# Kernel tuning notes

Hardware: AMD Instinct MI355X
Metric: run time of the kernel (lower is better)

The kernel has to match this reference:

```python
import jax, jax.numpy as jnp
import numpy as np

H = 128; W = 128; WH = 8; WW = 8; SH = 4; SW = 4
DIM = 512; HEADS = 16; HD = DIM // HEADS; HIDDEN = 2048
NH = H // WH; NW = W // WW; NWIN = NH * NW; WL = WH * WW
EPS = 1e-5
SCALE = HD ** -0.5


def _rel_pos_index():
    # Swin-style relative position index, static (WL, WL) int table
    coords = np.stack(np.meshgrid(np.arange(WH), np.arange(WW), indexing='ij')).reshape(2, -1)
    rel = (coords[:, :, None] - coords[:, None, :]).transpose(1, 2, 0)  # (WL, WL, 2)
    rel[:, :, 0] += WH - 1
    rel[:, :, 1] += WW - 1
    rel[:, :, 0] *= 2 * WW - 1
    return rel.sum(-1)  # (WL, WL), values in [0, (2WH-1)(2WW-1))


def _shift_attn_mask():
    # static shifted-window attention mask, (NWIN, WL, WL)
    m = np.zeros((H, W))
    cnt = 0
    for hs in (slice(0, -WH), slice(-WH, -SH), slice(-SH, None)):
        for ws in (slice(0, -WW), slice(-WW, -SW), slice(-SW, None)):
            m[hs, ws] = cnt
            cnt += 1
    mw = m.reshape(NH, WH, NW, WW).transpose(0, 2, 1, 3).reshape(NWIN, WL)
    am = mw[:, None, :] - mw[:, :, None]
    return np.where(am != 0, -100.0, 0.0).astype(np.float32)


_RPI = _rel_pos_index()
_MASK = _shift_attn_mask()


def _layernorm(x, w, b):
    mu = x.mean(-1, keepdims=True)
    var = ((x - mu) ** 2).mean(-1, keepdims=True)
    return (x - mu) / jnp.sqrt(var + EPS) * w + b


def _win_part(x):  # (H, W, D) -> (NWIN, WL, D)
    return x.reshape(NH, WH, NW, WW, DIM).transpose(0, 2, 1, 3, 4).reshape(NWIN, WL, DIM)


def _win_rev(w):  # (NWIN, WL, D) -> (H, W, D)
    return w.reshape(NH, NW, WH, WW, DIM).transpose(0, 2, 1, 3, 4).reshape(H, W, DIM)


def setup_inputs() -> dict:
    key = jax.random.key(0)
    ks = jax.random.split(key, 8)
    s = 0.02
    return {
        'x': jax.random.normal(ks[0], (H * W, DIM), dtype=jnp.float32),
        'ln1_w': jnp.ones((DIM,), jnp.float32),
        'ln1_b': jnp.zeros((DIM,), jnp.float32),
        'ln2_w': jnp.ones((DIM,), jnp.float32),
        'ln2_b': jnp.zeros((DIM,), jnp.float32),
        'qkv_w': jax.random.normal(ks[1], (3 * DIM, DIM), dtype=jnp.float32) * s,
        'qkv_b': jnp.zeros((3 * DIM,), jnp.float32),
        'proj_w': jax.random.normal(ks[2], (DIM, DIM), dtype=jnp.float32) * s,
        'proj_b': jnp.zeros((DIM,), jnp.float32),
        'rpb': jax.random.normal(ks[3], ((2 * WH - 1) * (2 * WW - 1), HEADS), dtype=jnp.float32) * s,
        'mlp_w1': jax.random.normal(ks[4], (HIDDEN, DIM), dtype=jnp.float32) * s,
        'mlp_b1': jnp.zeros((HIDDEN,), jnp.float32),
        'mlp_w2': jax.random.normal(ks[5], (DIM, HIDDEN), dtype=jnp.float32) * s,
        'mlp_b2': jnp.zeros((DIM,), jnp.float32),
    }


def reference(x, ln1_w, ln1_b, ln2_w, ln2_b, qkv_w, qkv_b, proj_w, proj_b, rpb,
              mlp_w1, mlp_b1, mlp_w2, mlp_b2):
    skip = x
    h = _layernorm(x, ln1_w, ln1_b).reshape(H, W, DIM)
    # cyclic shift + window partition
    h = jnp.roll(h, shift=(-SH, -SW), axis=(0, 1))
    xw = _win_part(h)  # (NWIN, WL, DIM)
    # windowed multi-head self-attention (equinox Linear: y = W @ x + b)
    qkv = jnp.einsum('nld,ed->nle', xw, qkv_w) + qkv_b
    q, k, v = [t.reshape(NWIN, WL, HEADS, HD).transpose(0, 2, 1, 3)
               for t in jnp.split(qkv, 3, axis=-1)]  # each (NWIN, HEADS, WL, HD)
    attn = jnp.einsum('nhqd,nhkd->nhqk', q * SCALE, k)
    bias = rpb[_RPI.reshape(-1)].reshape(WL, WL, HEADS).transpose(2, 0, 1)  # (HEADS, WL, WL)
    attn = attn + bias[None] + jnp.asarray(_MASK)[:, None]
    attn = jax.nn.softmax(attn, axis=-1)
    out = jnp.einsum('nhqk,nhkd->nhqd', attn, v).transpose(0, 2, 1, 3).reshape(NWIN, WL, DIM)
    out = jnp.einsum('nld,ed->nle', out, proj_w) + proj_b
    # window reverse + reverse cyclic shift
    h = jnp.roll(_win_rev(out), shift=(SH, SW), axis=(0, 1)).reshape(H * W, DIM)
    h = skip + h  # residual (drop_path is Identity at rate 0)
    # FFN branch (note: original code does x = x + drop_path(x), i.e. 2*mlp(norm2(.)))
    h = _layernorm(h, ln2_w, ln2_b)
    m = jax.nn.gelu(jnp.einsum('ld,ed->le', h, mlp_w1) + mlp_b1)
    m = jnp.einsum('le,de->ld', m, mlp_w2) + mlp_b2
    return m + m
```

## Files before the change

kernel.cpp:

```cpp
#include <hip/hip_runtime.h>
#include <hip/hip_bf16.h>
#include <stdint.h>

#define TOK   16384
#define DIMM  512
#define NHEAD 16
#define HDIM  32
#define HID   2048
#define NWIN  256
#define WLEN  64
#define EPSV  1e-5f
#define SCL   0.17677669529663687f

typedef __hip_bfloat16 bf16;
typedef __attribute__((ext_vector_type(8))) __bf16 bf16x8;
typedef __attribute__((ext_vector_type(4))) float f32x4;

__device__ __forceinline__ int remap_row(int r){
  int win = r >> 6, l = r & 63;
  int gh = ((win >> 4) << 3) + (l >> 3);
  int gw = ((win & 15) << 3) + (l & 7);
  int oh = (gh + 4) & 127, ow = (gw + 4) & 127;
  return (oh << 7) + ow;
}

__device__ __forceinline__ int region_of(int win, int l){
  int gh = ((win >> 4) << 3) + (l >> 3);
  int gw = ((win & 15) << 3) + (l & 7);
  int rh = (gh < 120) ? 0 : ((gh < 124) ? 1 : 2);
  int rw = (gw < 120) ? 0 : ((gw < 124) ? 1 : 2);
  return rh * 3 + rw;
}

__device__ __forceinline__ void gl_lds16(const bf16* g, bf16* l){
  __builtin_amdgcn_global_load_lds((const __attribute__((address_space(1))) void*)g,
                                   (__attribute__((address_space(3))) void*)l, 16, 0, 0);
}

__global__ __launch_bounds__(256) void convert_w(const float* __restrict__ a,
                                                 const float* __restrict__ b,
                                                 const float* __restrict__ c,
                                                 const float* __restrict__ d,
                                                 bf16* __restrict__ dst){
  int e = (blockIdx.x * 256 + threadIdx.x) * 4;
  float4 v;
  if (e < 786432)        v = *(const float4*)(a + e);
  else if (e < 1048576)  v = *(const float4*)(b + (e - 786432));
  else if (e < 2097152)  v = *(const float4*)(c + (e - 1048576));
  else                   v = *(const float4*)(d + (e - 2097152));
  union { bf16 h[4]; int2 q; } u;
  u.h[0] = __float2bfloat16(v.x); u.h[1] = __float2bfloat16(v.y);
  u.h[2] = __float2bfloat16(v.z); u.h[3] = __float2bfloat16(v.w);
  *(int2*)(dst + e) = u.q;
}

template<bool REMAP>
__global__ __launch_bounds__(256) void ln_kernel(const float* __restrict__ in,
    const float* __restrict__ w, const float* __restrict__ b, bf16* __restrict__ outp)
{
  const int wave = threadIdx.x >> 6, lane = threadIdx.x & 63;
  const int r = blockIdx.x * 4 + wave;
  const int src = REMAP ? remap_row(r) : r;
  const float4* row = (const float4*)(in + (size_t)src * DIMM);
  float4 v0 = row[lane*2], v1 = row[lane*2 + 1];
  float sm = v0.x+v0.y+v0.z+v0.w + v1.x+v1.y+v1.z+v1.w;
  float sq = v0.x*v0.x+v0.y*v0.y+v0.z*v0.z+v0.w*v0.w
           + v1.x*v1.x+v1.y*v1.y+v1.z*v1.z+v1.w*v1.w;
  #pragma unroll
  for (int off = 1; off < 64; off <<= 1){
    sm += __shfl_xor(sm, off);
    sq += __shfl_xor(sq, off);
  }
  const float mean = sm * (1.f/512.f);
  const float rstd = rsqrtf(sq*(1.f/512.f) - mean*mean + EPSV);
  const float4* wp = (const float4*)w; const float4* bp = (const float4*)b;
  float4 w0 = wp[lane*2], w1 = wp[lane*2+1], b0 = bp[lane*2], b1 = bp[lane*2+1];
  union { bf16 h[8]; int4 q; } u;
  u.h[0] = __float2bfloat16((v0.x-mean)*rstd*w0.x + b0.x);
  u.h[1] = __float2bfloat16((v0.y-mean)*rstd*w0.y + b0.y);
  u.h[2] = __float2bfloat16((v0.z-mean)*rstd*w0.z + b0.z);
  u.h[3] = __float2bfloat16((v0.w-mean)*rstd*w0.w + b0.w);
  u.h[4] = __float2bfloat16((v1.x-mean)*rstd*w1.x + b1.x);
  u.h[5] = __float2bfloat16((v1.y-mean)*rstd*w1.y + b1.y);
  u.h[6] = __float2bfloat16((v1.z-mean)*rstd*w1.z + b1.z);
  u.h[7] = __float2bfloat16((v1.w-mean)*rstd*w1.w + b1.w);
  *(int4*)(outp + (size_t)r*DIMM + lane*8) = u.q;
}

#define M_QKV  0
#define M_PROJ 1
#define M_MLP1 2
#define M_MLP2 3
#define M_PART 4

template<int MODE, int K>
__global__ __launch_bounds__(256) void gemm_bt(const bf16* __restrict__ A,
    const bf16* __restrict__ Wt, const float* __restrict__ bias,
    bf16* __restrict__ out_b, float* __restrict__ out_f, const float* __restrict__ skip)
{
  __shared__ bf16 lsA[2][128*32];
  __shared__ bf16 lsB[2][128*32];
  const int tid = threadIdx.x, wave = tid >> 6, lane = tid & 63;
  const int lrow = lane & 15, lgrp = lane >> 4;
  const int m0 = blockIdx.x * 128, n0 = blockIdx.y * 128;
  const int wr = (wave >> 1) * 64, wc = (wave & 1) * 64;

  f32x4 acc[4][4] = {};

  const bf16* Abase = A  + (size_t)m0 * K;
  const bf16* Bbase = Wt + (size_t)n0 * K;
  const int srow = tid >> 2;
  const int scol = (tid & 3) * 8;

  #define STAGE(kt, bf) { \
    gl_lds16(Abase + (size_t)(srow)      * K + (kt) + scol, lsA[bf] + wave*512); \
    gl_lds16(Abase + (size_t)(srow + 64) * K + (kt) + scol, lsA[bf] + 2048 + wave*512); \
    gl_lds16(Bbase + (size_t)(srow)      * K + (kt) + scol, lsB[bf] + wave*512); \
    gl_lds16(Bbase + (size_t)(srow + 64) * K + (kt) + scol, lsB[bf] + 2048 + wave*512); \
  }

  STAGE(0, 0);
  __syncthreads();
  int cur = 0;
  for (int kt = 0; kt < K; kt += 32){
    if (kt + 32 < K) STAGE(kt + 32, cur ^ 1);
    bf16x8 af[4], bfv[4];
    #pragma unroll
    for (int i = 0; i < 4; i++){
      af[i]  = *(const bf16x8*)(lsA[cur] + (wr + i*16 + lrow)*32 + lgrp*8);
      bfv[i] = *(const bf16x8*)(lsB[cur] + (wc + i*16 + lrow)*32 + lgrp*8);
    }
    #pragma unroll
    for (int i = 0; i < 4; i++)
      #pragma unroll
      for (int j = 0; j < 4; j++)
        acc[i][j] = __builtin_amdgcn_mfma_f32_16x16x32_bf16(af[i], bfv[j], acc[i][j], 0, 0, 0);
    __syncthreads();
    cur ^= 1;
  }
  #undef STAGE

  #pragma unroll
  for (int i = 0; i < 4; i++){
    #pragma unroll
    for (int j = 0; j < 4; j++){
      const int col   = n0 + wc + j*16 + lrow;
      const int row_b = m0 + wr + i*16 + lgrp*4;
      const float bv = bias[col];
      #pragma unroll
      for (int rr = 0; rr < 4; rr++){
        const int row = row_b + rr;
        float v = acc[i][j][rr] + bv;
        if constexpr (MODE == M_PROJ){
          const int o = remap_row(row);
          out_f[(size_t)o*DIMM + col] = v + skip[(size_t)o*DIMM + col];
        } else {
          out_f[(size_t)row*DIMM + col] = v;
        }
      }
    }
  }
}

template<int KSTR>
__device__ __forceinline__ void stage_ht(const bf16* __restrict__ P,
                                         int grow0, bf16* lbase, int tid, int kt){
  const int r = tid >> 3;
  const int c = ((tid & 7) ^ (r & 7)) * 8;
  const bf16* g = P + (size_t)(grow0 + r) * KSTR + kt * 64 + c;
  bf16* l = lbase + r * 64 + (tid & 7) * 8;
  gl_lds16(g, l);
  gl_lds16(g + (size_t)64 * KSTR, l + 4096);
}

template<int MODE, int KEXT, int KSTR = KEXT>
__global__ __launch_bounds__(512, 2) void gemm8_bt(const bf16* __restrict__ A,
    const bf16* __restrict__ Wt, const float* __restrict__ bias,
    bf16* __restrict__ out_b, float* __restrict__ out_f, float* __restrict__ out_f2)
{
  constexpr int NT = KEXT / 64;
  extern __shared__ bf16 lds[];
  bf16* As = lds;
  bf16* Bs = lds + 32768;
  const int tid = threadIdx.x;
  const int ln = tid & 63, wv = tid >> 6;
  const int lrow = ln & 15, lgrp = ln >> 4;
  const int swz = lrow & 7;
  const int wm = wv >> 2, wn = wv & 3;
  const int m0 = blockIdx.x * 256, n0 = blockIdx.y * 256;

  if constexpr (MODE == M_PART){
    const int z = blockIdx.z;
    A  += z * 1024;
    Wt += z * 1024;
  }

  f32x4 acc[8][4] = {};
  bf16x8 aA[4][2], bB0[2][2], bB1[2][2];

  #define LDA(MH) { _Pragma("unroll") for (int mf = 0; mf < 4; mf++) \
    _Pragma("unroll") for (int ks = 0; ks < 2; ks++) \
      aA[mf][ks] = *(const bf16x8*)(As + s*16384 + (wm*128 + (MH)*64 + mf*16 + lrow)*64 + ((ks*4 + lgrp) ^ swz)*8); }
  #define LDB(DST, NH) { _Pragma("unroll") for (int nf = 0; nf < 2; nf++) \
    _Pragma("unroll") for (int ks = 0; ks < 2; ks++) \
      DST[nf][ks] = *(const bf16x8*)(Bs + s*16384 + (wn*64 + (NH)*32 + nf*16 + lrow)*64 + ((ks*4 + lgrp) ^ swz)*8); }
  #define QUAD(BARR, IM0, JN0) { _Pragma("unroll") for (int ks = 0; ks < 2; ks++) \
    _Pragma("unroll") for (int mf = 0; mf < 4; mf++) \
      _Pragma("unroll") for (int nf = 0; nf < 2; nf++) \
        acc[(IM0)+mf][(JN0)+nf] = __builtin_amdgcn_mfma_f32_16x16x32_bf16(aA[mf][ks], BARR[nf][ks], acc[(IM0)+mf][(JN0)+nf], 0, 0, 0); }
  #define SBAR() { __builtin_amdgcn_sched_barrier(0); __builtin_amdgcn_s_barrier(); __builtin_amdgcn_sched_barrier(0); }
  #define LGKM0() { asm volatile("s_waitcnt lgkmcnt(0)" ::: "memory"); __builtin_amdgcn_sched_barrier(0); }

  stage_ht<KSTR>(A,  m0,       As,        tid, 0);
  stage_ht<KSTR>(Wt, n0,       Bs,        tid, 0);
  stage_ht<KSTR>(Wt, n0 + 128, Bs + 8192, tid, 0);
  stage_ht<KSTR>(A,  m0 + 128, As + 8192, tid, 0);
  asm volatile("s_waitcnt vmcnt(0)" ::: "memory");
  SBAR();
  stage_ht<KSTR>(Wt, n0,       Bs + 16384,        tid, 1);
  stage_ht<KSTR>(A,  m0,       As + 16384,        tid, 1);
  stage_ht<KSTR>(Wt, n0 + 128, Bs + 16384 + 8192, tid, 1);

  for (int t = 0; t < NT; ++t){
    const int s = t & 1;
    const int sx = s ^ 1;
    LDA(0); LDB(bB0, 0);
    if (t + 1 < NT) stage_ht<KSTR>(A, m0 + 128, As + sx*16384 + 8192, tid, t + 1);
    SBAR(); LGKM0();
    __builtin_amdgcn_s_setprio(1); QUAD(bB0, 0, 0); __builtin_amdgcn_s_setprio(0);
    SBAR();
    LDB(bB1, 1);
    SBAR(); LGKM0();
    __builtin_amdgcn_s_setprio(1); QUAD(bB1, 0, 2); __builtin_amdgcn_s_setprio(0);
    SBAR();
    LDA(1);
    if (t + 2 < NT) stage_ht<KSTR>(Wt, n0, Bs + s*16384, tid, t + 2);
    SBAR(); LGKM0();
    __builtin_amdgcn_s_setprio(1); QUAD(bB1, 4, 2); __builtin_amdgcn_s_setprio(0);
    SBAR();
    if (t + 2 < NT){
      stage_ht<KSTR>(A,  m0,       As + s*16384,        tid, t + 2);
      stage_ht<KSTR>(Wt, n0 + 128, Bs + s*16384 + 8192, tid, t + 2);
    }
    SBAR();
    __builtin_amdgcn_s_setprio(1); QUAD(bB0, 4, 0); __builtin_amdgcn_s_setprio(0);
    if (t == NT - 2)      { asm volatile("s_waitcnt vmcnt(0)" ::: "memory"); }
    else if (t < NT - 2)  { asm volatile("s_waitcnt vmcnt(6)" ::: "memory"); }
    SBAR();
  }
  #undef LDA
  #undef LDB
  #undef QUAD
  #undef SBAR
  #undef LGKM0

  float* pdst = nullptr;
  if constexpr (MODE == M_PART) pdst = blockIdx.z ? out_f2 : out_f;
  #pragma unroll
  for (int im = 0; im < 8; im++){
    #pragma unroll
    for (int jn = 0; jn < 4; jn++){
      const int col = n0 + wn*64 + (jn >> 1)*32 + (jn & 1)*16 + lrow;
      const int row_b = m0 + wm*128 + (im >> 2)*64 + (im & 3)*16 + lgrp*4;
      const float bv = (MODE == M_PART) ? 0.f : bias[col];
      #pragma unroll
      for (int rr = 0; rr < 4; rr++){
        const int row = row_b + rr;
        float v = acc[im][jn][rr] + bv;
        if constexpr (MODE == M_QKV){
          const int t = col >> 9, rem = col & 511;
          const int head = rem >> 5, hd = rem & 31;
          const int win = row >> 6, l = row & 63;
          out_b[(size_t)t * (TOK*DIMM) + ((size_t)(win*NHEAD + head)*WLEN + l)*HDIM + hd]
              = __float2bfloat16(v);
        } else if constexpr (MODE == M_MLP1){
          const float u = 1.5957691216057308f * (v + 0.044715f*v*v*v);
          const float g = v * (1.0f / (1.0f + __expf(-u)));
          out_b[(size_t)row*HID + col] = __float2bfloat16(g);
        } else if constexpr (MODE == M_PART){
          pdst[(size_t)row*DIMM + col] = v;
        } else {
          out_f[(size_t)row*DIMM + col] = 2.f * v;
        }
      }
    }
  }
}

__global__ __launch_bounds__(256) void mlp2_reduce(const float* __restrict__ p0,
    float* __restrict__ dout, const float* __restrict__ bias){
  const int i = blockIdx.x * 256 + threadIdx.x;
  const int e = i * 4;
  float4 a = *(const float4*)(p0 + e);
  float4 b = *(const float4*)(dout + e);
  float4 bv = *(const float4*)(bias + (e & 511));
  float4 r;
  r.x = 2.f*(a.x + b.x + bv.x);
  r.y = 2.f*(a.y + b.y + bv.y);
  r.z = 2.f*(a.z + b.z + bv.z);
  r.w = 2.f*(a.w + b.w + bv.w);
  *(float4*)(dout + e) = r;
}

__global__ __launch_bounds__(256) void attn_kernel(const bf16* __restrict__ qkv,
    const float* __restrict__ rpb, bf16* __restrict__ outp)
{
  __shared__ bf16 Pl[4][64][72];
  const int wave = threadIdx.x >> 6, lane = threadIdx.x & 63;
  const int lrow = lane & 15, lgrp = lane >> 4;
  const int wh = blockIdx.x * 4 + wave;
  const int win = wh >> 4, head = wh & 15;
  const bf16* qb = qkv + (size_t)wh * (WLEN*HDIM);
  const bf16* kb = qb + (size_t)TOK * DIMM;
  const bf16* vb = kb + (size_t)TOK * DIMM;

  bf16x8 aq[4], ak[4];
  #pragma unroll
  for (int i = 0; i < 4; i++){
    aq[i] = *(const bf16x8*)(qb + (i*16 + lrow)*HDIM + lgrp*8);
    ak[i] = *(const bf16x8*)(kb + (i*16 + lrow)*HDIM + lgrp*8);
  }
  f32x4 s[4][4] = {};
  #pragma unroll
  for (int i = 0; i < 4; i++)
    #pragma unroll
    for (int j = 0; j < 4; j++)
      s[i][j] = __builtin_amdgcn_mfma_f32_16x16x32_bf16(aq[i], ak[j], s[i][j], 0, 0, 0);

  #pragma unroll
  for (int i = 0; i < 4; i++){
    #pragma unroll
    for (int rr = 0; rr < 4; rr++){
      const int srow = i*16 + lgrp*4 + rr;
      const int rq = region_of(win, srow);
      float vals[4]; float mx = -1e30f;
      #pragma unroll
      for (int j = 0; j < 4; j++){
        const int scol = j*16 + lrow;
        const int idx = ((srow>>3) - (scol>>3) + 7)*15 + ((srow&7) - (scol&7) + 7);
        float v = s[i][j][rr]*SCL + rpb[idx*NHEAD + head];
        if (region_of(win, scol) != rq) v -= 100.f;
        vals[j] = v; mx = fmaxf(mx, v);
      }
      mx = fmaxf(mx, __shfl_xor(mx, 1));
      mx = fmaxf(mx, __shfl_xor(mx, 2));
      mx = fmaxf(mx, __shfl_xor(mx, 4));
      mx = fmaxf(mx, __shfl_xor(mx, 8));
      float sum = 0.f;
      #pragma unroll
      for (int j = 0; j < 4; j++){ vals[j] = __expf(vals[j] - mx); sum += vals[j]; }
      sum += __shfl_xor(sum, 1); sum += __shfl_xor(sum, 2);
      sum += __shfl_xor(sum, 4); sum += __shfl_xor(sum, 8);
      const float rs = 1.f / sum;
      #pragma unroll
      for (int j = 0; j < 4; j++)
        Pl[wave][srow][j*16 + lrow] = __float2bfloat16(vals[j] * rs);
    }
  }

  f32x4 o[4][2] = {};
  const __bf16* vraw = (const __bf16*)vb;
  #pragma unroll
  for (int st = 0; st < 2; st++){
    bf16x8 pa[4];
    #pragma unroll
    for (int i = 0; i < 4; i++)
      pa[i] = *(const bf16x8*)(&Pl[wave][i*16 + lrow][st*32 + lgrp*8]);
    bf16x8 bv[2];
    #pragma unroll
    for (int j = 0; j < 2; j++){
      #pragma unroll
      for (int jj = 0; jj < 8; jj++)
        bv[j][jj] = vraw[(size_t)(st*32 + lgrp*8 + jj)*HDIM + j*16 + lrow];
    }
    #pragma unroll
    for (int i = 0; i < 4; i++)
      #pragma unroll
      for (int j = 0; j < 2; j++)
        o[i][j] = __builtin_amdgcn_mfma_f32_16x16x32_bf16(pa[i], bv[j], o[i][j], 0, 0, 0);
  }
  bf16* orow = outp + (size_t)win * WLEN * DIMM + head * HDIM;
  #pragma unroll
  for (int i = 0; i < 4; i++)
    #pragma unroll
    for (int j = 0; j < 2; j++)
      #pragma unroll
      for (int rr = 0; rr < 4; rr++){
        const int l = i*16 + lgrp*4 + rr;
        orow[(size_t)l * DIMM + j*16 + lrow] = __float2bfloat16(o[i][j][rr]);
      }
}

extern "C" void kernel_launch(void* const* d_in, const int* in_sizes, int n_in,
                              void* d_out, int out_size, void* d_ws, size_t ws_size,
                              hipStream_t stream) {
  const float* x     = (const float*)d_in[0];
  const float* ln1w  = (const float*)d_in[1];
  const float* ln1b  = (const float*)d_in[2];
  const float* ln2w  = (const float*)d_in[3];
  const float* ln2b  = (const float*)d_in[4];
  const float* qkvw  = (const float*)d_in[5];
  const float* qkvbi = (const float*)d_in[6];
  const float* projw = (const float*)d_in[7];
  const float* projb = (const float*)d_in[8];
  const float* rpb   = (const float*)d_in[9];
  const float* m1w   = (const float*)d_in[10];
  const float* m1b   = (const float*)d_in[11];
  const float* m2w   = (const float*)d_in[12];
  const float* m2b   = (const float*)d_in[13];

  bf16* wqkv  = (bf16*)d_ws;
  bf16* wproj = wqkv + 786432;
  bf16* wm1   = wproj + 262144;
  bf16* wm2   = wm1 + 1048576;
  bf16* xw    = wm2 + 1048576;
  float* hbuf = (float*)(xw + 8388608);
  bf16* qkvb  = (bf16*)(hbuf + 8388608);
  bf16* attno = qkvb + 3*(size_t)8388608;
  bf16* m1buf = qkvb;
  bf16* h2    = xw;

  hipFuncSetAttribute((const void*)&gemm8_bt<M_QKV, 512>,
                      hipFuncAttributeMaxDynamicSharedMemorySize, 131072);
  hipFuncSetAttribute((const void*)&gemm8_bt<M_MLP1, 512>,
                      hipFuncAttributeMaxDynamicSharedMemorySize, 131072);
  hipFuncSetAttribute((const void*)&gemm8_bt<M_PART, 1024, 2048>,
                      hipFuncAttributeMaxDynamicSharedMemorySize, 131072);

  convert_w<<<3072, 256, 0, stream>>>(qkvw, projw, m1w, m2w, wqkv);
  ln_kernel<true><<<4096, 256, 0, stream>>>(x, ln1w, ln1b, xw);
  { dim3 g(TOK/256, 1536/256);
    gemm8_bt<M_QKV, 512><<<g, 512, 131072, stream>>>(xw, wqkv, qkvbi, qkvb, nullptr, nullptr); }
  attn_kernel<<<1024, 256, 0, stream>>>(qkvb, rpb, attno);
  { dim3 g(TOK/128, 512/128);
    gemm_bt<M_PROJ, 512><<<g, 256, 0, stream>>>(attno, wproj, projb, nullptr, hbuf, x); }
  ln_kernel<false><<<4096, 256, 0, stream>>>(hbuf, ln2w, ln2b, h2);
  { dim3 g(TOK/256, 2048/256);
    gemm8_bt<M_MLP1, 512><<<g, 512, 131072, stream>>>(h2, wm1, m1b, m1buf, nullptr, nullptr); }
  { dim3 g(TOK/256, 512/256, 2);
    gemm8_bt<M_PART, 1024, 2048><<<g, 512, 131072, stream>>>(m1buf, wm2, m2b, nullptr,
                                                             hbuf, (float*)d_out); }
  mlp2_reduce<<<8388608/4/256, 256, 0, stream>>>(hbuf, (float*)d_out, m2b);
}
```

Baseline: 229.6 us.

## Store MLP2 split-K partials in bf16 and drop redundant GEMM barriers

The split-K partial sums of the second MLP GEMM are now written as bf16 into scratch buffers instead of fp32, and the reduce kernel reads two bf16 partials and writes fp32 output. This roughly halves the partial-write and reduce-read traffic at the cost of precision in the partial sums. Separately, several workgroup barriers before the LDS-wait/MFMA sections in the gemm8 main loop are removed to cut synchronisation stalls. Removing those barriers risks LDS races if the remaining barriers do not fully order staging against reads.

```diff
diff --git a/kernel.cpp b/kernel.cpp
--- a/kernel.cpp
+++ b/kernel.cpp
@@ -226,23 +226,22 @@
     const int sx = s ^ 1;
     LDA(0); LDB(bB0, 0);
     if (t + 1 < NT) stage_ht<KSTR>(A, m0 + 128, As + sx*16384 + 8192, tid, t + 1);
-    SBAR(); LGKM0();
+    LGKM0();
     __builtin_amdgcn_s_setprio(1); QUAD(bB0, 0, 0); __builtin_amdgcn_s_setprio(0);
     SBAR();
     LDB(bB1, 1);
-    SBAR(); LGKM0();
+    LGKM0();
     __builtin_amdgcn_s_setprio(1); QUAD(bB1, 0, 2); __builtin_amdgcn_s_setprio(0);
     SBAR();
     LDA(1);
     if (t + 2 < NT) stage_ht<KSTR>(Wt, n0, Bs + s*16384, tid, t + 2);
-    SBAR(); LGKM0();
+    LGKM0();
     __builtin_amdgcn_s_setprio(1); QUAD(bB1, 4, 2); __builtin_amdgcn_s_setprio(0);
     SBAR();
     if (t + 2 < NT){
       stage_ht<KSTR>(A,  m0,       As + s*16384,        tid, t + 2);
       stage_ht<KSTR>(Wt, n0 + 128, Bs + s*16384 + 8192, tid, t + 2);
     }
-    SBAR();
     __builtin_amdgcn_s_setprio(1); QUAD(bB0, 4, 0); __builtin_amdgcn_s_setprio(0);
     if (t == NT - 2)      { asm volatile("s_waitcnt vmcnt(0)" ::: "memory"); }
     else if (t < NT - 2)  { asm volatile("s_waitcnt vmcnt(6)" ::: "memory"); }
@@ -254,8 +253,9 @@
   #undef SBAR
   #undef LGKM0
 
-  float* pdst = nullptr;
-  if constexpr (MODE == M_PART) pdst = blockIdx.z ? out_f2 : out_f;
+  bf16* pdstb = nullptr;
+  if constexpr (MODE == M_PART)
+    pdstb = blockIdx.z ? (bf16*)out_f2 : (bf16*)out_f;
   #pragma unroll
   for (int im = 0; im < 8; im++){
     #pragma unroll
@@ -278,7 +278,7 @@
           const float g = v * (1.0f / (1.0f + __expf(-u)));
           out_b[(size_t)row*HID + col] = __float2bfloat16(g);
         } else if constexpr (MODE == M_PART){
-          pdst[(size_t)row*DIMM + col] = v;
+          pdstb[(size_t)row*DIMM + col] = __float2bfloat16(v);
         } else {
           out_f[(size_t)row*DIMM + col] = 2.f * v;
         }
@@ -287,19 +287,27 @@
   }
 }
 
-__global__ __launch_bounds__(256) void mlp2_reduce(const float* __restrict__ p0,
-    float* __restrict__ dout, const float* __restrict__ bias){
-  const int i = blockIdx.x * 256 + threadIdx.x;
-  const int e = i * 4;
-  float4 a = *(const float4*)(p0 + e);
-  float4 b = *(const float4*)(dout + e);
-  float4 bv = *(const float4*)(bias + (e & 511));
-  float4 r;
-  r.x = 2.f*(a.x + b.x + bv.x);
-  r.y = 2.f*(a.y + b.y + bv.y);
-  r.z = 2.f*(a.z + b.z + bv.z);
-  r.w = 2.f*(a.w + b.w + bv.w);
-  *(float4*)(dout + e) = r;
+__global__ __launch_bounds__(256) void mlp2_reduce(const bf16* __restrict__ p0,
+    const bf16* __restrict__ p1, float* __restrict__ dout, const float* __restrict__ bias){
+  const size_t i = (size_t)(blockIdx.x * 256 + threadIdx.x) * 8;
+  int4 a = *(const int4*)(p0 + i);
+  int4 b = *(const int4*)(p1 + i);
+  const int cb = (int)(i & 511);
+  const float4 bv0 = *(const float4*)(bias + cb);
+  const float4 bv1 = *(const float4*)(bias + cb + 4);
+  const bf16* ah = (const bf16*)&a;
+  const bf16* bh = (const bf16*)&b;
+  float4 r0, r1;
+  r0.x = 2.f*(__bfloat162float(ah[0]) + __bfloat162float(bh[0]) + bv0.x);
+  r0.y = 2.f*(__bfloat162float(ah[1]) + __bfloat162float(bh[1]) + bv0.y);
+  r0.z = 2.f*(__bfloat162float(ah[2]) + __bfloat162float(bh[2]) + bv0.z);
+  r0.w = 2.f*(__bfloat162float(ah[3]) + __bfloat162float(bh[3]) + bv0.w);
+  r1.x = 2.f*(__bfloat162float(ah[4]) + __bfloat162float(bh[4]) + bv1.x);
+  r1.y = 2.f*(__bfloat162float(ah[5]) + __bfloat162float(bh[5]) + bv1.y);
+  r1.z = 2.f*(__bfloat162float(ah[6]) + __bfloat162float(bh[6]) + bv1.z);
+  r1.w = 2.f*(__bfloat162float(ah[7]) + __bfloat162float(bh[7]) + bv1.w);
+  *(float4*)(dout + i)     = r0;
+  *(float4*)(dout + i + 4) = r1;
 }
 
 __global__ __launch_bounds__(256) void attn_kernel(const bf16* __restrict__ qkv,
@@ -439,6 +447,7 @@
     gemm8_bt<M_MLP1, 512><<<g, 512, 131072, stream>>>(h2, wm1, m1b, m1buf, nullptr, nullptr); }
   { dim3 g(TOK/256, 512/256, 2);
     gemm8_bt<M_PART, 1024, 2048><<<g, 512, 131072, stream>>>(m1buf, wm2, m2b, nullptr,
-                                                             hbuf, (float*)d_out); }
-  mlp2_reduce<<<8388608/4/256, 256, 0, stream>>>(hbuf, (float*)d_out, m2b);
-}
+                                                             (float*)hbuf, (float*)xw); }
+  mlp2_reduce<<<8388608/8/256, 256, 0, stream>>>((const bf16*)hbuf, (const bf16*)xw,
+                                                 (float*)d_out, m2b);
+}
```

Result: faster. 222.6 us (-3.0%).
